# Kernel optimization log

Measured on AMD Instinct MI355X. Metric: run time of the kernel, lower is better.

Reference implementation:

```python
import jax, jax.numpy as jnp
import numpy as np


def setup_inputs() -> dict:
    key = jax.random.key(0)
    k1, k2 = jax.random.split(key)
    B, S, D, R = 8, 2048, 1024, 128
    batch = jax.random.normal(k1, (B, S, D), dtype=jnp.float32)
    proj = jax.random.normal(k2, (D, R), dtype=jnp.float32) * (1.0 / np.sqrt(D))
    return {"batch": batch, "proj": proj}


def reference(batch, proj):
    # transformed: (B, S, R)
    t = jnp.matmul(batch, proj)
    # Pairwise squared L2 distances: ||ti||^2 + ||tj||^2 - 2 ti.tj
    # (same math as expand/diff/pow/sum, without the (B,S,S,R) intermediate)
    sq = jnp.sum(t * t, axis=-1)                       # (B, S)
    dots = jnp.einsum('bir,bjr->bij', t, t)            # (B, S, S)
    d2 = sq[:, :, None] + sq[:, None, :] - 2.0 * dots  # (B, S, S)
    return d2
```

## Files before the change

kernel.cpp:

```cpp
#include <hip/hip_runtime.h>
#include <hip/hip_bf16.h>

typedef short bf16x8 __attribute__((ext_vector_type(8)));
typedef float f32x4 __attribute__((ext_vector_type(4)));

#define NB 8
#define SS 2048
#define DD 1024
#define RR 128

__device__ __forceinline__ short f2bf(float x){
  unsigned u = __float_as_uint(x);
  u += 0x7fffu + ((u >> 16) & 1u);
  return (short)(u >> 16);
}
__device__ __forceinline__ float bf2f(short h){
  return __uint_as_float(((unsigned)(unsigned short)h) << 16);
}
__device__ __forceinline__ void gload16(const void* g, void* l){
  __builtin_amdgcn_global_load_lds((const __attribute__((address_space(1))) unsigned*)g,
                                   (__attribute__((address_space(3))) unsigned*)l, 16, 0, 0);
}
__device__ __forceinline__ int swz(int row, int c16){
  return row * 64 + ((c16 ^ (row & 7)) << 3);
}

__global__ __launch_bounds__(256) void k0_proj(const float* __restrict__ proj,
                                               short* __restrict__ pt_hi,
                                               short* __restrict__ pt_lo){
  __shared__ float tile[64][65];
  const int d0 = blockIdx.x * 64, r0 = blockIdx.y * 64;
  const int tid = threadIdx.x;
  #pragma unroll
  for (int i = 0; i < 16; ++i){
    int u = i * 256 + tid;
    int d = u >> 6, r = u & 63;
    tile[d][r] = proj[(d0 + d) * RR + r0 + r];
  }
  __syncthreads();
  #pragma unroll
  for (int i = 0; i < 16; ++i){
    int u = i * 256 + tid;
    int r = u >> 6, d = u & 63;
    float x = tile[d][r];
    short h = f2bf(x);
    short l = f2bf(x - bf2f(h));
    pt_hi[(r0 + r) * DD + d0 + d] = h;
    pt_lo[(r0 + r) * DD + d0 + d] = l;
  }
}

__global__ __launch_bounds__(512, 2) void k1_gemm1(const float* __restrict__ batch,
                                                   const short* __restrict__ pt_hi,
                                                   const short* __restrict__ pt_lo,
                                                   short* __restrict__ t_hi,
                                                   short* __restrict__ t_lo,
                                                   float* __restrict__ sqv){
  __shared__ __align__(16) char smem[49408];
  short* Ah = (short*)smem;
  short* Al = (short*)(smem + 8192);
  short* Ph = (short*)(smem + 16384);
  short* Pl = (short*)(smem + 32768);
  float* sqpart = (float*)(smem + 49152);
  const int tid = threadIdx.x;
  const int w = tid >> 6, lane = tid & 63;
  const int lr = lane & 15, lg = lane >> 4;
  const int wr = w & 3, wc = w >> 2;
  const int row0 = blockIdx.x * 64;
  const int colg = (lane & 7) ^ (lane >> 3);
  if (tid < 64) sqpart[tid] = 0.f;
  f32x4 acc[4] = {{0.f,0.f,0.f,0.f}};
  #pragma unroll 1
  for (int k0 = 0; k0 < DD; k0 += 64){
    #pragma unroll
    for (int i = 0; i < 2; ++i){
      int u = tid * 2 + i;
      int r = u >> 4, kc = (u & 15) * 4;
      float4 v = *(const float4*)(batch + (size_t)(row0 + r) * DD + k0 + kc);
      short4 hv, lv;
      hv.x = f2bf(v.x); lv.x = f2bf(v.x - bf2f(hv.x));
      hv.y = f2bf(v.y); lv.y = f2bf(v.y - bf2f(hv.y));
      hv.z = f2bf(v.z); lv.z = f2bf(v.z - bf2f(hv.z));
      hv.w = f2bf(v.w); lv.w = f2bf(v.w - bf2f(hv.w));
      int sidx = r * 64 + (((kc >> 3) ^ (r & 7)) << 3) + (kc & 7);
      *(short4*)&Ah[sidx] = hv;
      *(short4*)&Al[sidx] = lv;
    }
    #pragma unroll
    for (int q = 0; q < 2; ++q){
      int prow = w * 16 + q * 8 + (lane >> 3);
      const short* gh = pt_hi + prow * DD + k0 + colg * 8;
      const short* gl = pt_lo + prow * DD + k0 + colg * 8;
      gload16(gh, &Ph[w * 1024 + q * 512]);
      gload16(gl, &Pl[w * 1024 + q * 512]);
    }
    __syncthreads();
    #pragma unroll
    for (int ks = 0; ks < 2; ++ks){
      int c16 = ks * 4 + lg;
      bf16x8 ah = *(const bf16x8*)&Ah[swz(wr * 16 + lr, c16)];
      bf16x8 al = *(const bf16x8*)&Al[swz(wr * 16 + lr, c16)];
      bf16x8 bh[4], bl[4];
      #pragma unroll
      for (int n = 0; n < 4; ++n){
        int prow = wc * 64 + n * 16 + lr;
        bh[n] = *(const bf16x8*)&Ph[swz(prow, c16)];
        bl[n] = *(const bf16x8*)&Pl[swz(prow, c16)];
      }
      #pragma unroll
      for (int n = 0; n < 4; ++n)
        acc[n] = __builtin_amdgcn_mfma_f32_16x16x32_bf16(ah, bh[n], acc[n], 0, 0, 0);
      #pragma unroll
      for (int n = 0; n < 4; ++n)
        acc[n] = __builtin_amdgcn_mfma_f32_16x16x32_bf16(ah, bl[n], acc[n], 0, 0, 0);
      #pragma unroll
      for (int n = 0; n < 4; ++n)
        acc[n] = __builtin_amdgcn_mfma_f32_16x16x32_bf16(al, bh[n], acc[n], 0, 0, 0);
    }
    __syncthreads();
  }
  short* Th = Ph;
  short* Tl = Pl;
  #pragma unroll
  for (int r = 0; r < 4; ++r){
    int lrow = wr * 16 + lg * 4 + r;
    float s = 0.f;
    #pragma unroll
    for (int n = 0; n < 4; ++n){
      float x = acc[n][r];
      s += x * x;
      int col = wc * 64 + n * 16 + lr;
      short h = f2bf(x);
      short l = f2bf(x - bf2f(h));
      Th[lrow * 128 + col] = h;
      Tl[lrow * 128 + col] = l;
    }
    s += __shfl_xor(s, 1);
    s += __shfl_xor(s, 2);
    s += __shfl_xor(s, 4);
    s += __shfl_xor(s, 8);
    if (lr == 0) atomicAdd(&sqpart[lrow], s);
  }
  __syncthreads();
  #pragma unroll
  for (int ps = 0; ps < 2; ++ps){
    int u = ps * 512 + tid;
    int row = u >> 4, c8 = (u & 15) * 8;
    *(int4*)&t_hi[(size_t)(row0 + row) * RR + c8] = *(int4*)&Th[row * 128 + c8];
    *(int4*)&t_lo[(size_t)(row0 + row) * RR + c8] = *(int4*)&Tl[row * 128 + c8];
  }
  if (tid < 64) sqv[row0 + tid] = sqpart[tid];
}

__global__ __launch_bounds__(256, 2) void k2_dist(const short* __restrict__ t_hi,
                                                  const short* __restrict__ t_lo,
                                                  const float* __restrict__ sqv,
                                                  float* __restrict__ out){
  __shared__ __align__(16) char smem[65536];
  short* Ah = (short*)smem;
  short* Al = (short*)(smem + 16384);
  short* Bh = (short*)(smem + 32768);
  short* Bl = (short*)(smem + 49152);
  float* ftile = (float*)smem;
  const int tid = threadIdx.x;
  const int w = tid >> 6, lane = tid & 63;
  const int lr = lane & 15, lg = lane >> 4;
  const int bi = blockIdx.x;
  int p = blockIdx.y;
  int ti = 0;
  while (p >= 16 - ti){ p -= 16 - ti; ++ti; }
  const int tj = ti + p;
  const int i0 = ti * 128, j0 = tj * 128;
  const size_t tbase = (size_t)bi * SS * RR;
  const int colg = (lane & 7) ^ (lane >> 3);

  f32x4 acc[16] = {{0.f,0.f,0.f,0.f}};
  #pragma unroll 1
  for (int k0 = 0; k0 < RR; k0 += 64){
    #pragma unroll
    for (int q = 0; q < 4; ++q){
      int rloc = w * 32 + q * 8 + (lane >> 3);
      size_t goffA = tbase + (size_t)(i0 + rloc) * RR + k0 + colg * 8;
      size_t goffB = tbase + (size_t)(j0 + rloc) * RR + k0 + colg * 8;
      int ldst = w * 2048 + q * 512;
      gload16(t_hi + goffA, &Ah[ldst]);
      gload16(t_lo + goffA, &Al[ldst]);
      gload16(t_hi + goffB, &Bh[ldst]);
      gload16(t_lo + goffB, &Bl[ldst]);
    }
    __syncthreads();
    #pragma unroll
    for (int ks = 0; ks < 2; ++ks){
      int c16 = ks * 4 + lg;
      bf16x8 ah[2], al[2];
      #pragma unroll
      for (int rt = 0; rt < 2; ++rt){
        int arow = w * 32 + rt * 16 + lr;
        ah[rt] = *(const bf16x8*)&Ah[swz(arow, c16)];
        al[rt] = *(const bf16x8*)&Al[swz(arow, c16)];
      }
      bf16x8 bh[8], bl[8];
      #pragma unroll
      for (int n = 0; n < 8; ++n){
        int brow = n * 16 + lr;
        bh[n] = *(const bf16x8*)&Bh[swz(brow, c16)];
        bl[n] = *(const bf16x8*)&Bl[swz(brow, c16)];
      }
      #pragma unroll
      for (int rt = 0; rt < 2; ++rt)
        #pragma unroll
        for (int n = 0; n < 8; ++n)
          acc[rt * 8 + n] = __builtin_amdgcn_mfma_f32_16x16x32_bf16(ah[rt], bh[n], acc[rt * 8 + n], 0, 0, 0);
      #pragma unroll
      for (int rt = 0; rt < 2; ++rt)
        #pragma unroll
        for (int n = 0; n < 8; ++n)
          acc[rt * 8 + n] = __builtin_amdgcn_mfma_f32_16x16x32_bf16(ah[rt], bl[n], acc[rt * 8 + n], 0, 0, 0);
      #pragma unroll
      for (int rt = 0; rt < 2; ++rt)
        #pragma unroll
        for (int n = 0; n < 8; ++n)
          acc[rt * 8 + n] = __builtin_amdgcn_mfma_f32_16x16x32_bf16(al[rt], bh[n], acc[rt * 8 + n], 0, 0, 0);
    }
    __syncthreads();
  }
  float* outb = out + (size_t)bi * SS * SS;
  const float* sqb = sqv + bi * SS;
  #pragma unroll
  for (int rt = 0; rt < 2; ++rt)
    #pragma unroll
    for (int n = 0; n < 8; ++n)
      #pragma unroll
      for (int r = 0; r < 4; ++r)
        ftile[(w * 32 + rt * 16 + lg * 4 + r) * 128 + n * 16 + lr] = acc[rt * 8 + n][r];
  __syncthreads();
  #pragma unroll
  for (int v = 0; v < 16; ++v){
    int u = v * 256 + tid;
    int row = u >> 5, c4 = (u & 31) * 4;
    float4 d = *(float4*)&ftile[row * 128 + c4];
    float si = sqb[i0 + row];
    float4 sj = *(const float4*)&sqb[j0 + c4];
    float4 o;
    o.x = si + sj.x - 2.0f * d.x;
    o.y = si + sj.y - 2.0f * d.y;
    o.z = si + sj.z - 2.0f * d.z;
    o.w = si + sj.w - 2.0f * d.w;
    *(float4*)&outb[(size_t)(i0 + row) * SS + j0 + c4] = o;
  }
  if (ti != tj){
    #pragma unroll
    for (int rt = 0; rt < 2; ++rt){
      int rbase = w * 32 + rt * 16 + lg * 4;
      float4 si4 = *(const float4*)&sqb[i0 + rbase];
      #pragma unroll
      for (int n = 0; n < 8; ++n){
        int col = n * 16 + lr;
        float sj = sqb[j0 + col];
        float4 mv;
        mv.x = si4.x + sj - 2.0f * acc[rt * 8 + n][0];
        mv.y = si4.y + sj - 2.0f * acc[rt * 8 + n][1];
        mv.z = si4.z + sj - 2.0f * acc[rt * 8 + n][2];
        mv.w = si4.w + sj - 2.0f * acc[rt * 8 + n][3];
        *(float4*)&outb[(size_t)(j0 + col) * SS + i0 + rbase] = mv;
      }
    }
  }
}

extern "C" void kernel_launch(void* const* d_in, const int* in_sizes, int n_in,
                              void* d_out, int out_size, void* d_ws, size_t ws_size,
                              hipStream_t stream) {
  const float* batch = (const float*)d_in[0];
  const float* proj  = (const float*)d_in[1];
  float* out = (float*)d_out;
  char* ws = (char*)d_ws;

  short* pt_hi = (short*)(ws);
  short* pt_lo = (short*)(ws + 262144);
  short* t_hi  = (short*)(ws + 524288);
  short* t_lo  = (short*)(ws + 4718592);
  float* sqv   = (float*)(ws + 8912896);

  k0_proj<<<dim3(16, 2), 256, 0, stream>>>(proj, pt_hi, pt_lo);
  k1_gemm1<<<dim3(256), 512, 0, stream>>>(batch, pt_hi, pt_lo, t_hi, t_lo, sqv);
  k2_dist<<<dim3(8, 136), 256, 0, stream>>>(t_hi, t_lo, sqv, out);
}
```

Measured before the change: 215.3 us.

## Make distance kernel persistent with full-K staging and prefetch overlapped with stores

The distance kernel becomes a persistent grid of 256 blocks with 512 threads. Each block walks through upper-triangle tiles with a stride of 32. The whole K=128 slice is staged in LDS at once, and diagonal tiles load only the A operand. The next tile's global-to-LDS load is issued before the current tile's output stores, so loads overlap the write phase. The LDS-transposed coalesced store is replaced by direct scalar stores for the direct tile, which risks less coalesced writes on the dominant 134MB output stream.

New measurement: 214.5 us. No clear change (-0.3%).

```diff
diff --git a/kernel.cpp b/kernel.cpp
--- a/kernel.cpp
+++ b/kernel.cpp
@@ -152,119 +152,105 @@
   if (tid < 64) sqv[row0 + tid] = sqpart[tid];
 }
 
-__global__ __launch_bounds__(256, 2) void k2_dist(const short* __restrict__ t_hi,
+__global__ __launch_bounds__(512, 1) void k2_dist(const short* __restrict__ t_hi,
                                                   const short* __restrict__ t_lo,
                                                   const float* __restrict__ sqv,
                                                   float* __restrict__ out){
-  __shared__ __align__(16) char smem[65536];
-  short* Ah = (short*)smem;
-  short* Al = (short*)(smem + 16384);
-  short* Bh = (short*)(smem + 32768);
-  short* Bl = (short*)(smem + 49152);
-  float* ftile = (float*)smem;
+  __shared__ short lds[65536];
   const int tid = threadIdx.x;
   const int w = tid >> 6, lane = tid & 63;
   const int lr = lane & 15, lg = lane >> 4;
-  const int bi = blockIdx.x;
-  int p = blockIdx.y;
-  int ti = 0;
-  while (p >= 16 - ti){ p -= 16 - ti; ++ti; }
-  const int tj = ti + p;
-  const int i0 = ti * 128, j0 = tj * 128;
+  const int srow = ((w & 1) << 2) | (lane >> 4);
+  const int colg = (lane & 15) ^ srow;
+  const int bi = blockIdx.x & 7;
+  const int lidx = blockIdx.x >> 3;
   const size_t tbase = (size_t)bi * SS * RR;
-  const int colg = (lane & 7) ^ (lane >> 3);
-
-  f32x4 acc[16] = {{0.f,0.f,0.f,0.f}};
-  #pragma unroll 1
-  for (int k0 = 0; k0 < RR; k0 += 64){
-    #pragma unroll
-    for (int q = 0; q < 4; ++q){
-      int rloc = w * 32 + q * 8 + (lane >> 3);
-      size_t goffA = tbase + (size_t)(i0 + rloc) * RR + k0 + colg * 8;
-      size_t goffB = tbase + (size_t)(j0 + rloc) * RR + k0 + colg * 8;
-      int ldst = w * 2048 + q * 512;
-      gload16(t_hi + goffA, &Ah[ldst]);
-      gload16(t_lo + goffA, &Al[ldst]);
-      gload16(t_hi + goffB, &Bh[ldst]);
-      gload16(t_lo + goffB, &Bl[ldst]);
-    }
-    __syncthreads();
-    #pragma unroll
-    for (int ks = 0; ks < 2; ++ks){
-      int c16 = ks * 4 + lg;
-      bf16x8 ah[2], al[2];
-      #pragma unroll
-      for (int rt = 0; rt < 2; ++rt){
-        int arow = w * 32 + rt * 16 + lr;
-        ah[rt] = *(const bf16x8*)&Ah[swz(arow, c16)];
-        al[rt] = *(const bf16x8*)&Al[swz(arow, c16)];
-      }
-      bf16x8 bh[8], bl[8];
-      #pragma unroll
-      for (int n = 0; n < 8; ++n){
-        int brow = n * 16 + lr;
-        bh[n] = *(const bf16x8*)&Bh[swz(brow, c16)];
-        bl[n] = *(const bf16x8*)&Bl[swz(brow, c16)];
-      }
-      #pragma unroll
-      for (int rt = 0; rt < 2; ++rt)
-        #pragma unroll
-        for (int n = 0; n < 8; ++n)
-          acc[rt * 8 + n] = __builtin_amdgcn_mfma_f32_16x16x32_bf16(ah[rt], bh[n], acc[rt * 8 + n], 0, 0, 0);
-      #pragma unroll
-      for (int rt = 0; rt < 2; ++rt)
-        #pragma unroll
-        for (int n = 0; n < 8; ++n)
-          acc[rt * 8 + n] = __builtin_amdgcn_mfma_f32_16x16x32_bf16(ah[rt], bl[n], acc[rt * 8 + n], 0, 0, 0);
-      #pragma unroll
-      for (int rt = 0; rt < 2; ++rt)
-        #pragma unroll
-        for (int n = 0; n < 8; ++n)
-          acc[rt * 8 + n] = __builtin_amdgcn_mfma_f32_16x16x32_bf16(al[rt], bh[n], acc[rt * 8 + n], 0, 0, 0);
-    }
-    __syncthreads();
-  }
   float* outb = out + (size_t)bi * SS * SS;
   const float* sqb = sqv + bi * SS;
-  #pragma unroll
-  for (int rt = 0; rt < 2; ++rt)
-    #pragma unroll
-    for (int n = 0; n < 8; ++n)
-      #pragma unroll
-      for (int r = 0; r < 4; ++r)
-        ftile[(w * 32 + rt * 16 + lg * 4 + r) * 128 + n * 16 + lr] = acc[rt * 8 + n][r];
-  __syncthreads();
-  #pragma unroll
-  for (int v = 0; v < 16; ++v){
-    int u = v * 256 + tid;
-    int row = u >> 5, c4 = (u & 31) * 4;
-    float4 d = *(float4*)&ftile[row * 128 + c4];
-    float si = sqb[i0 + row];
-    float4 sj = *(const float4*)&sqb[j0 + c4];
-    float4 o;
-    o.x = si + sj.x - 2.0f * d.x;
-    o.y = si + sj.y - 2.0f * d.y;
-    o.z = si + sj.z - 2.0f * d.z;
-    o.w = si + sj.w - 2.0f * d.w;
-    *(float4*)&outb[(size_t)(i0 + row) * SS + j0 + c4] = o;
-  }
-  if (ti != tj){
-    #pragma unroll
-    for (int rt = 0; rt < 2; ++rt){
-      int rbase = w * 32 + rt * 16 + lg * 4;
+
+  auto decodeP = [&](int p, int& i0, int& j0, bool& dg){
+    int ti = 0;
+    while (p >= 16 - ti){ p -= 16 - ti; ++ti; }
+    int tj = ti + p;
+    i0 = ti * 128; j0 = tj * 128; dg = (ti == tj);
+  };
+  auto stageTile = [&](int i0, int j0, bool dg){
+    #pragma unroll
+    for (int q = 0; q < 4; ++q){
+      int rl = q * 32 + w * 4;
+      int gr = rl + (lane >> 4);
+      size_t oA = tbase + (size_t)(i0 + gr) * RR + colg * 8;
+      gload16(t_hi + oA, &lds[rl * 128]);
+      gload16(t_lo + oA, &lds[16384 + rl * 128]);
+      if (!dg){
+        size_t oB = tbase + (size_t)(j0 + gr) * RR + colg * 8;
+        gload16(t_hi + oB, &lds[32768 + rl * 128]);
+        gload16(t_lo + oB, &lds[49152 + rl * 128]);
+      }
+    }
+  };
+
+  int p = lidx;
+  int i0, j0; bool dg;
+  decodeP(p, i0, j0, dg);
+  stageTile(i0, j0, dg);
+  while (true){
+    __syncthreads();
+    const int bh0 = dg ? 0 : 32768, bl0 = dg ? 16384 : 49152;
+    f32x4 acc[8] = {{0.f,0.f,0.f,0.f}};
+    const int ar = w * 16 + lr;
+    const int aoff = ar * 128;
+    const int asw = (ar & 7);
+    #pragma unroll
+    for (int ks = 0; ks < 4; ++ks){
+      int c16 = ks * 4 + lg;
+      bf16x8 ah = *(const bf16x8*)&lds[aoff + ((c16 ^ asw) << 3)];
+      bf16x8 al = *(const bf16x8*)&lds[16384 + aoff + ((c16 ^ asw) << 3)];
+      bf16x8 bh[8], bl[8];
+      #pragma unroll
+      for (int n = 0; n < 8; ++n){
+        int br = n * 16 + lr;
+        int off = br * 128 + ((c16 ^ (br & 7)) << 3);
+        bh[n] = *(const bf16x8*)&lds[bh0 + off];
+        bl[n] = *(const bf16x8*)&lds[bl0 + off];
+      }
+      #pragma unroll
+      for (int n = 0; n < 8; ++n)
+        acc[n] = __builtin_amdgcn_mfma_f32_16x16x32_bf16(ah, bh[n], acc[n], 0, 0, 0);
+      #pragma unroll
+      for (int n = 0; n < 8; ++n)
+        acc[n] = __builtin_amdgcn_mfma_f32_16x16x32_bf16(ah, bl[n], acc[n], 0, 0, 0);
+      #pragma unroll
+      for (int n = 0; n < 8; ++n)
+        acc[n] = __builtin_amdgcn_mfma_f32_16x16x32_bf16(al, bh[n], acc[n], 0, 0, 0);
+    }
+    __syncthreads();
+    int np = p + 32;
+    bool more = (np < 136);
+    int ni0, nj0; bool ndg;
+    if (more){ decodeP(np, ni0, nj0, ndg); stageTile(ni0, nj0, ndg); }
+    {
+      int rbase = w * 16 + lg * 4;
       float4 si4 = *(const float4*)&sqb[i0 + rbase];
       #pragma unroll
       for (int n = 0; n < 8; ++n){
         int col = n * 16 + lr;
         float sj = sqb[j0 + col];
-        float4 mv;
-        mv.x = si4.x + sj - 2.0f * acc[rt * 8 + n][0];
-        mv.y = si4.y + sj - 2.0f * acc[rt * 8 + n][1];
-        mv.z = si4.z + sj - 2.0f * acc[rt * 8 + n][2];
-        mv.w = si4.w + sj - 2.0f * acc[rt * 8 + n][3];
-        *(float4*)&outb[(size_t)(j0 + col) * SS + i0 + rbase] = mv;
-      }
-    }
+        float4 v;
+        v.x = si4.x + sj - 2.0f * acc[n][0];
+        v.y = si4.y + sj - 2.0f * acc[n][1];
+        v.z = si4.z + sj - 2.0f * acc[n][2];
+        v.w = si4.w + sj - 2.0f * acc[n][3];
+        size_t ro = (size_t)(i0 + rbase) * SS + (j0 + col);
+        outb[ro] = v.x;
+        outb[ro + SS] = v.y;
+        outb[ro + 2 * SS] = v.z;
+        outb[ro + 3 * SS] = v.w;
+        if (!dg) *(float4*)&outb[(size_t)(j0 + col) * SS + (i0 + rbase)] = v;
+      }
+    }
+    if (!more) break;
+    p = np; i0 = ni0; j0 = nj0; dg = ndg;
   }
 }
 
@@ -284,5 +270,5 @@
 
   k0_proj<<<dim3(16, 2), 256, 0, stream>>>(proj, pt_hi, pt_lo);
   k1_gemm1<<<dim3(256), 512, 0, stream>>>(batch, pt_hi, pt_lo, t_hi, t_lo, sqv);
-  k2_dist<<<dim3(8, 136), 256, 0, stream>>>(t_hi, t_lo, sqv, out);
-}
+  k2_dist<<<dim3(256), 512, 0, stream>>>(t_hi, t_lo, sqv, out);
+}
```
